# Performance work log

Hardware: AMD Instinct MI355X
Metric: run time of the kernel (lower is better)

The kernel has to match this reference:

```python
import jax, jax.numpy as jnp
import numpy as np

B, S, D_IN, D_H = 4, 2048, 1024, 1024


def setup_inputs() -> dict:
    key = jax.random.key(0)
    k1, k2, k3, k4, k5, k6 = jax.random.split(key, 6)
    seq1 = jax.random.normal(k1, (B, S, D_IN), dtype=jnp.float32)
    seq2 = jax.random.normal(k2, (B, S, D_IN), dtype=jnp.float32)
    attn_mask = jax.random.randint(k3, (B, S, S), 0, 2).astype(jnp.bool_)
    # nn.Linear weights: shape [out, in], y = x @ W^T
    scale = 1.0 / np.sqrt(D_IN)
    Wq = jax.random.uniform(k4, (D_H, D_IN), dtype=jnp.float32, minval=-scale, maxval=scale)
    Wk = jax.random.uniform(k5, (D_H, D_IN), dtype=jnp.float32, minval=-scale, maxval=scale)
    Wv = jax.random.uniform(k6, (D_H, D_IN), dtype=jnp.float32, minval=-scale, maxval=scale)
    return {"seq1": seq1, "seq2": seq2, "attn_mask": attn_mask, "Wq": Wq, "Wk": Wk, "Wv": Wv}


def reference(seq1, seq2, attn_mask, Wq, Wk, Wv):
    q = jnp.einsum('bsd,hd->bsh', seq1, Wq)
    k = jnp.einsum('bsd,hd->bsh', seq2, Wk)
    v = jnp.einsum('bsd,hd->bsh', seq2, Wv)
    score = jnp.einsum('bqh,bkh->bqk', q, k) / jnp.sqrt(jnp.float32(q.shape[-1]))
    # faithful to torch.masked_fill(..., value=1e-09): masked positions set to 1e-9
    mask_score = jnp.where(attn_mask, jnp.float32(1e-09), score)
    # faithful to torch.softmax(..., dim=1): softmax over the QUERY axis
    score_matrix = jax.nn.softmax(mask_score, axis=1)
    out = jnp.einsum('bqk,bkh->bqh', score_matrix, v)
    return out
```

## Files before the change

### kernel.cpp

```cpp
#include <hip/hip_runtime.h>

typedef __bf16 bx8 __attribute__((ext_vector_type(8)));
typedef __bf16 bx4 __attribute__((ext_vector_type(4)));
typedef float  fx4 __attribute__((ext_vector_type(4)));
typedef unsigned long long u64;

#define B_   4
#define S_   2048
#define DIN  1024
#define DH   1024

#define MB ((size_t)1 << 20)
#define WS_A1 ((size_t)0)
#define WS_A2 ((size_t)16*MB)
#define WS_PU ((size_t)0)
#define WS_WQ ((size_t)32*MB)
#define WS_BM ((size_t)38*MB)
#define WS_Q  ((size_t)40*MB)
#define WS_K  ((size_t)56*MB)
#define WS_VT ((size_t)72*MB)
#define WS_CS ((size_t)88*MB)

__global__ void cvt_seq(const float* __restrict__ s1, const float* __restrict__ s2,
                        __bf16* __restrict__ o1, __bf16* __restrict__ o2) {
  const float* in  = blockIdx.y ? s2 : s1;
  __bf16*      out = blockIdx.y ? o2 : o1;
  size_t i = (size_t)blockIdx.x * blockDim.x + threadIdx.x;
  fx4 lo = ((const fx4*)in)[2 * i];
  fx4 hi = ((const fx4*)in)[2 * i + 1];
  bx8 o;
#pragma unroll
  for (int j = 0; j < 4; j++) { o[j] = (__bf16)lo[j]; o[j + 4] = (__bf16)hi[j]; }
  ((bx8*)out)[i] = o;
}
__global__ void cvt_w(const float* __restrict__ wq, const float* __restrict__ wk,
                      const float* __restrict__ wv, __bf16* __restrict__ oq) {
  const float* in = blockIdx.y == 0 ? wq : (blockIdx.y == 1 ? wk : wv);
  __bf16* out = oq + (size_t)blockIdx.y * (DH * DIN);
  size_t i = (size_t)blockIdx.x * blockDim.x + threadIdx.x;
  fx4 lo = ((const fx4*)in)[2 * i];
  fx4 hi = ((const fx4*)in)[2 * i + 1];
  bx8 o;
#pragma unroll
  for (int j = 0; j < 4; j++) { o[j] = (__bf16)lo[j]; o[j + 4] = (__bf16)hi[j]; }
  ((bx8*)out)[i] = o;
}

__global__ void pack_mask(const int* __restrict__ m, u64* __restrict__ w) {
  const int wid = threadIdx.x >> 6, lane = threadIdx.x & 63;
  const size_t base = ((size_t)blockIdx.x * 4 + wid) * 512;
#pragma unroll
  for (int i = 0; i < 8; i++) {
    int v = m[base + i * 64 + lane];
    u64 b = __ballot(v != 0);
    if (lane == 0) w[base / 64 + i] = b;
  }
}


enum { EP_QKV = 0, EP_EXP = 2, EP_F32 = 3 };

#define GLD(gp, lp)                                                              \
  __builtin_amdgcn_global_load_lds(                                              \
      (const __attribute__((address_space(1))) void*)(const void*)(gp),          \
      (__attribute__((address_space(3))) void*)(void*)(lp), 16, 0, 0)

#define ENDSYNC()                                          \
  do {                                                     \
    asm volatile("s_waitcnt vmcnt(0)" ::: "memory");       \
    __builtin_amdgcn_s_barrier();                          \
    __builtin_amdgcn_sched_barrier(0);                     \
  } while (0)

#define MM(m, n, av, bv) \
  acc[m][n] = __builtin_amdgcn_mfma_f32_16x16x32_bf16(av, bv, acc[m][n], 0, 0, 0)

#define LDA_(bo, m, kk) (*(const bx8*)(aBase + (bo) + (m) * 2048 + ((kk) ? c1s : c0s)))
#define LDB_(bo, n, kk) (*(const bx8*)(bBase + (bo) + (n) * 2048 + ((kk) ? c1s : c0s)))

#define STAGE_A(kt, bo) do {                                              \
  GLD(pA + (kt),                    smem + (bo) + tid * 16);              \
  GLD(pA + (size_t)64 * K + (kt),   smem + (bo) + 8192 + tid * 16);       \
} while (0)
#define STAGE_B(kt, bo) do {                                              \
  GLD(pB + (kt),                    smem + (bo) + 16384 + tid * 16);      \
  GLD(pB + (size_t)64 * K + (kt),   smem + (bo) + 24576 + tid * 16);      \
} while (0)

template <int EPI>
__global__ __launch_bounds__(512, 4) void gemm128(
    const __bf16* __restrict__ A, const __bf16* __restrict__ Bm,
    void* __restrict__ Cout, void* __restrict__ Cout2,
    const void* __restrict__ Xtra, int N, int K, long sA, long sB) {
  extern __shared__ char smem[];

  int brow, bcol, bz = 0, qrow = 0;
  bool isQ = false;
  if (EPI == EP_QKV) {
    int f = (blockIdx.x & 7) * 192 + (blockIdx.x >> 3);
    if (f < 512) {
      isQ = true;
      qrow = (f >> 3) * 128;
      brow = qrow;
      bcol = (f & 7) * 128;
    } else {
      int g = f - 512;
      qrow = (g >> 4) * 128;
      brow = 8192 + qrow;
      bcol = (g & 15) * 128;
    }
  } else {
    const unsigned gx = gridDim.x, gy = gridDim.y;
    const unsigned nwg = gx * gy * gridDim.z;
    unsigned flat = (blockIdx.z * gy + blockIdx.y) * gx + blockIdx.x;
    flat = (flat & 7) * (nwg >> 3) + (flat >> 3);
    const int lx = __builtin_ctz(gx), ly = __builtin_ctz(gy);
    brow = ((flat >> lx) & (gy - 1)) * 128;
    bcol = (flat & (gx - 1)) * 128;
    bz   = flat >> (lx + ly);
    A  += (long)bz * sA;
    Bm += (long)bz * sB;
  }

  const int tid  = threadIdx.x;
  const int wid  = tid >> 6;
  const int lane = tid & 63;
  const int wr = wid >> 2;
  const int wc = wid & 3;

  fx4 acc[4][2] = {};

  const int gcol = (((tid & 7) ^ ((tid >> 3) & 7)) << 3);
  const __bf16* Bsel = (EPI == EP_QKV && !isQ) ? (Bm + (size_t)1048576) : Bm;
  const __bf16* pA = A    + (size_t)(brow + (tid >> 3)) * K + gcol;
  const __bf16* pB = Bsel + (size_t)(bcol + (tid >> 3)) * K + gcol;

  const int frow = lane & 15;
  const int slot = (lane >> 4) << 4;
  const int c0s  = slot ^ ((frow & 7) << 4);
  const int c1s  = (64 + slot) ^ ((frow & 7) << 4);
  const char* aBase = smem + (wr * 64 + frow) * 128;
  const char* bBase = smem + 16384 + (wc * 32 + frow) * 128;

  STAGE_A(0, 0); STAGE_B(0, 0);
  ENDSYNC();

  const int nt = K >> 6;
  int cur = 0, nb = 32768;
  bx8 a00, a01, a02, a03, a10, a11, a12, a13, b00, b01, b10, b11;

  for (int t = 0; t < nt; ++t) {
    const int k1 = (t + 1 < nt) ? (t + 1) * 64 : 0;

    STAGE_A(k1, nb); STAGE_B(k1, nb);

    a00 = LDA_(cur, 0, 0); a01 = LDA_(cur, 1, 0); a02 = LDA_(cur, 2, 0); a03 = LDA_(cur, 3, 0);
    b00 = LDB_(cur, 0, 0); b01 = LDB_(cur, 1, 0);
    a10 = LDA_(cur, 0, 1); a11 = LDA_(cur, 1, 1); a12 = LDA_(cur, 2, 1); a13 = LDA_(cur, 3, 1);
    b10 = LDB_(cur, 0, 1); b11 = LDB_(cur, 1, 1);

    __builtin_amdgcn_s_setprio(1);
    MM(0, 0, a00, b00); MM(0, 1, a00, b01);
    MM(1, 0, a01, b00); MM(1, 1, a01, b01);
    MM(2, 0, a02, b00); MM(2, 1, a02, b01);
    MM(3, 0, a03, b00); MM(3, 1, a03, b01);
    MM(0, 0, a10, b10); MM(0, 1, a10, b11);
    MM(1, 0, a11, b10); MM(1, 1, a11, b11);
    MM(2, 0, a12, b10); MM(2, 1, a12, b11);
    MM(3, 0, a13, b10); MM(3, 1, a13, b11);
    __builtin_amdgcn_s_setprio(0);

    ENDSYNC();
    int tmp = cur; cur = nb; nb = tmp;
  }

  const int r0 = wr * 64 + (lane >> 4) * 4;
  const int c0 = wc * 32 + (lane & 15);

  if (EPI == EP_QKV) {
    if (isQ) {
      __bf16* Cq = (__bf16*)Cout;
#pragma unroll
      for (int m = 0; m < 4; m++) {
        int row = qrow + r0 + m * 16;
#pragma unroll
        for (int n = 0; n < 2; n++) {
          int col = bcol + c0 + n * 16;
#pragma unroll
          for (int j = 0; j < 4; j++)
            Cq[(size_t)(row + j) * 1024 + col] = (__bf16)acc[m][n][j];
        }
      }
    } else if (bcol < 1024) {
      __bf16* Ck = (__bf16*)Cout2;
#pragma unroll
      for (int m = 0; m < 4; m++) {
        int rr = qrow + r0 + m * 16;
#pragma unroll
        for (int n = 0; n < 2; n++) {
          int col = bcol + c0 + n * 16;
#pragma unroll
          for (int j = 0; j < 4; j++)
            Ck[(size_t)(rr + j) * 1024 + col] = (__bf16)acc[m][n][j];
        }
      }
    } else {
      __bf16* Cv = (__bf16*)Xtra;
#pragma unroll
      for (int m = 0; m < 4; m++) {
        int rr = qrow + r0 + m * 16;
        size_t bb = (size_t)(rr >> 11) << 21;
        int sidx = rr & 2047;
#pragma unroll
        for (int n = 0; n < 2; n++) {
          int col = bcol + c0 + n * 16 - 1024;
          bx4 tv;
#pragma unroll
          for (int j = 0; j < 4; j++) tv[j] = (__bf16)acc[m][n][j];
          *(bx4*)&Cv[bb + (size_t)col * S_ + sidx] = tv;
        }
      }
    }
  } else if (EPI == EP_EXP) {
    __bf16* C     = (__bf16*)Cout + (size_t)bz * ((size_t)S_ * S_);
    const u64* Wm = (const u64*)Xtra + (((size_t)bz * S_ * S_) >> 6);
    float csum0 = 0.f, csum1 = 0.f;
#pragma unroll
    for (int m = 0; m < 4; m++) {
      int row = brow + r0 + m * 16;
#pragma unroll
      for (int n = 0; n < 2; n++) {
        int col = bcol + c0 + n * 16;
        float cl = 0.f;
#pragma unroll
        for (int j = 0; j < 4; j++) {
          size_t idx = (size_t)(row + j) * S_ + col;
          bool mk = (Wm[idx >> 6] >> (idx & 63)) & 1;
          float p = mk ? 1.0f : __expf(acc[m][n][j] * 0.03125f);
          cl += p;
          C[idx] = (__bf16)p;
        }
        if (n == 0) csum0 += cl; else csum1 += cl;
      }
    }
    csum0 += __shfl_xor(csum0, 16); csum0 += __shfl_xor(csum0, 32);
    csum1 += __shfl_xor(csum1, 16); csum1 += __shfl_xor(csum1, 32);
    if (lane < 16) {
      float* csp = (float*)Cout2 + (size_t)bz * S_ + bcol + wc * 32 + lane;
      atomicAdd(csp, csum0);
      atomicAdd(csp + 16, csum1);
    }
  } else {
    float* C = (float*)Cout + (size_t)bz * ((size_t)S_ * DH);
#pragma unroll
    for (int m = 0; m < 4; m++) {
      int row = brow + r0 + m * 16;
#pragma unroll
      for (int n = 0; n < 2; n++) {
        int col = bcol + c0 + n * 16;
#pragma unroll
        for (int j = 0; j < 4; j++)
          C[(size_t)(row + j) * N + col] = acc[m][n][j];
      }
    }
  }
}

__global__ void scale_vt(__bf16* __restrict__ vT, const float* __restrict__ cs) {
  size_t i = (size_t)blockIdx.x * blockDim.x + threadIdx.x;
  size_t e = i * 8;
  int b = (int)(e >> 21);
  int k = (int)(e & (S_ - 1));
  bx8 v = ((bx8*)vT)[i];
  const float* c = cs + (size_t)b * S_ + k;
#pragma unroll
  for (int j = 0; j < 8; j++) v[j] = (__bf16)((float)v[j] / c[j]);
  ((bx8*)vT)[i] = v;
}

extern "C" void kernel_launch(void* const* d_in, const int* in_sizes, int n_in,
                              void* d_out, int out_size, void* d_ws, size_t ws_size,
                              hipStream_t stream) {
  const float* seq1 = (const float*)d_in[0];
  const float* seq2 = (const float*)d_in[1];
  const int*   mask = (const int*)d_in[2];
  const float* Wq   = (const float*)d_in[3];
  const float* Wk   = (const float*)d_in[4];
  const float* Wv   = (const float*)d_in[5];

  char* ws = (char*)d_ws;
  __bf16* A1  = (__bf16*)(ws + WS_A1);
  __bf16* A2  = (__bf16*)(ws + WS_A2);
  __bf16* Pu  = (__bf16*)(ws + WS_PU);
  __bf16* WQb = (__bf16*)(ws + WS_WQ);
  u64*    bm  = (u64*)(ws + WS_BM);
  __bf16* qb  = (__bf16*)(ws + WS_Q);
  __bf16* kb  = (__bf16*)(ws + WS_K);
  __bf16* vTb = (__bf16*)(ws + WS_VT);
  float*  cs  = (float*)(ws + WS_CS);

  (void)hipFuncSetAttribute((const void*)gemm128<EP_QKV>,
      hipFuncAttributeMaxDynamicSharedMemorySize, 65536);
  (void)hipFuncSetAttribute((const void*)gemm128<EP_EXP>,
      hipFuncAttributeMaxDynamicSharedMemorySize, 65536);
  (void)hipFuncSetAttribute((const void*)gemm128<EP_F32>,
      hipFuncAttributeMaxDynamicSharedMemorySize, 65536);

  cvt_seq<<<dim3(4096, 2, 1), 256, 0, stream>>>(seq1, seq2, A1, A2);
  cvt_w<<<dim3(512, 3, 1), 256, 0, stream>>>(Wq, Wk, Wv, WQb);
  pack_mask<<<8192, 256, 0, stream>>>(mask, bm);
  hipMemsetAsync(ws + WS_CS, 0, (size_t)B_ * S_ * sizeof(float), stream);

  gemm128<EP_QKV><<<1536, 512, 65536, stream>>>(
      A1, WQb, qb, kb, vTb, 0, DIN, 0, 0);

  gemm128<EP_EXP><<<dim3(S_ / 128, S_ / 128, B_), 512, 65536, stream>>>(
      qb, kb, Pu, cs, bm, S_, DH, (long)S_ * DH, (long)S_ * DH);

  scale_vt<<<(B_ * DH * S_ / 8) / 256, 256, 0, stream>>>(vTb, cs);

  gemm128<EP_F32><<<dim3(DH / 128, S_ / 128, B_), 512, 65536, stream>>>(
      Pu, vTb, (float*)d_out, nullptr, nullptr, DH, S_, (long)S_ * S_, (long)DH * S_);
}
```

Before: 178.9 us.

## Fuse fp32-to-bf16 activation conversion and V column scaling into GEMM loaders

Removes the standalone cvt_seq and scale_vt kernels. The QKV GEMM now loads fp32 seq1/seq2 through registers, converts them to bf16 and writes them into LDS. The PV GEMM loads vT into registers, scales it by the reciprocal column sums, converts and stores it into LDS. This drops two extra passes over global memory and two launches. In exchange, those loads no longer use async global-to-LDS, they read twice the bytes for the A operand, and the loop waits on lgkmcnt, which may lengthen each iteration.

```diff
diff --git a/kernel.cpp b/kernel.cpp
--- a/kernel.cpp
+++ b/kernel.cpp
@@ -11,8 +11,6 @@
 #define DH   1024
 
 #define MB ((size_t)1 << 20)
-#define WS_A1 ((size_t)0)
-#define WS_A2 ((size_t)16*MB)
 #define WS_PU ((size_t)0)
 #define WS_WQ ((size_t)32*MB)
 #define WS_BM ((size_t)38*MB)
@@ -21,18 +19,6 @@
 #define WS_VT ((size_t)72*MB)
 #define WS_CS ((size_t)88*MB)
 
-__global__ void cvt_seq(const float* __restrict__ s1, const float* __restrict__ s2,
-                        __bf16* __restrict__ o1, __bf16* __restrict__ o2) {
-  const float* in  = blockIdx.y ? s2 : s1;
-  __bf16*      out = blockIdx.y ? o2 : o1;
-  size_t i = (size_t)blockIdx.x * blockDim.x + threadIdx.x;
-  fx4 lo = ((const fx4*)in)[2 * i];
-  fx4 hi = ((const fx4*)in)[2 * i + 1];
-  bx8 o;
-#pragma unroll
-  for (int j = 0; j < 4; j++) { o[j] = (__bf16)lo[j]; o[j + 4] = (__bf16)hi[j]; }
-  ((bx8*)out)[i] = o;
-}
 __global__ void cvt_w(const float* __restrict__ wq, const float* __restrict__ wk,
                       const float* __restrict__ wv, __bf16* __restrict__ oq) {
   const float* in = blockIdx.y == 0 ? wq : (blockIdx.y == 1 ? wk : wv);
@@ -65,11 +51,11 @@
       (const __attribute__((address_space(1))) void*)(const void*)(gp),          \
       (__attribute__((address_space(3))) void*)(void*)(lp), 16, 0, 0)
 
-#define ENDSYNC()                                          \
-  do {                                                     \
-    asm volatile("s_waitcnt vmcnt(0)" ::: "memory");       \
-    __builtin_amdgcn_s_barrier();                          \
-    __builtin_amdgcn_sched_barrier(0);                     \
+#define ENDSYNC()                                                      \
+  do {                                                                 \
+    asm volatile("s_waitcnt vmcnt(0) lgkmcnt(0)" ::: "memory");        \
+    __builtin_amdgcn_s_barrier();                                      \
+    __builtin_amdgcn_sched_barrier(0);                                 \
   } while (0)
 
 #define MM(m, n, av, bv) \
@@ -78,11 +64,11 @@
 #define LDA_(bo, m, kk) (*(const bx8*)(aBase + (bo) + (m) * 2048 + ((kk) ? c1s : c0s)))
 #define LDB_(bo, n, kk) (*(const bx8*)(bBase + (bo) + (n) * 2048 + ((kk) ? c1s : c0s)))
 
-#define STAGE_A(kt, bo) do {                                              \
+#define STAGE_A_GLD(kt, bo) do {                                          \
   GLD(pA + (kt),                    smem + (bo) + tid * 16);              \
   GLD(pA + (size_t)64 * K + (kt),   smem + (bo) + 8192 + tid * 16);       \
 } while (0)
-#define STAGE_B(kt, bo) do {                                              \
+#define STAGE_B_GLD(kt, bo) do {                                          \
   GLD(pB + (kt),                    smem + (bo) + 16384 + tid * 16);      \
   GLD(pB + (size_t)64 * K + (kt),   smem + (bo) + 24576 + tid * 16);      \
 } while (0)
@@ -91,7 +77,8 @@
 __global__ __launch_bounds__(512, 4) void gemm128(
     const __bf16* __restrict__ A, const __bf16* __restrict__ Bm,
     void* __restrict__ Cout, void* __restrict__ Cout2,
-    const void* __restrict__ Xtra, int N, int K, long sA, long sB) {
+    const void* __restrict__ Xtra, const float* __restrict__ F1,
+    const float* __restrict__ F2, int N, int K, long sA, long sB) {
   extern __shared__ char smem[];
 
   int brow, bcol, bz = 0, qrow = 0;
@@ -101,14 +88,13 @@
     if (f < 512) {
       isQ = true;
       qrow = (f >> 3) * 128;
-      brow = qrow;
       bcol = (f & 7) * 128;
     } else {
       int g = f - 512;
       qrow = (g >> 4) * 128;
-      brow = 8192 + qrow;
       bcol = (g & 15) * 128;
     }
+    brow = qrow;
   } else {
     const unsigned gx = gridDim.x, gy = gridDim.y;
     const unsigned nwg = gx * gy * gridDim.z;
@@ -132,8 +118,11 @@
 
   const int gcol = (((tid & 7) ^ ((tid >> 3) & 7)) << 3);
   const __bf16* Bsel = (EPI == EP_QKV && !isQ) ? (Bm + (size_t)1048576) : Bm;
-  const __bf16* pA = A    + (size_t)(brow + (tid >> 3)) * K + gcol;
-  const __bf16* pB = Bsel + (size_t)(bcol + (tid >> 3)) * K + gcol;
+  const __bf16* pA  = A    + (size_t)(brow + (tid >> 3)) * K + gcol;
+  const __bf16* pB  = Bsel + (size_t)(bcol + (tid >> 3)) * K + gcol;
+  const float*  pAf = (EPI == EP_QKV ? (isQ ? F1 : F2) : nullptr)
+                      + ((EPI == EP_QKV) ? ((size_t)(qrow + (tid >> 3)) * DIN + gcol) : 0);
+  const float*  csb = (EPI == EP_F32) ? (F1 + (size_t)bz * S_) : nullptr;
 
   const int frow = lane & 15;
   const int slot = (lane >> 4) << 4;
@@ -142,17 +131,63 @@
   const char* aBase = smem + (wr * 64 + frow) * 128;
   const char* bBase = smem + 16384 + (wc * 32 + frow) * 128;
 
-  STAGE_A(0, 0); STAGE_B(0, 0);
-  ENDSYNC();
-
   const int nt = K >> 6;
   int cur = 0, nb = 32768;
   bx8 a00, a01, a02, a03, a10, a11, a12, a13, b00, b01, b10, b11;
+  fx4 fa0, fa1, fa2, fa3;
+  bx8 lv0, lv1;
+  fx4 cs0, cs1;
+
+  if (EPI == EP_QKV) {
+    fa0 = *(const fx4*)(pAf);       fa1 = *(const fx4*)(pAf + 4);
+    fa2 = *(const fx4*)(pAf + (size_t)64 * DIN);
+    fa3 = *(const fx4*)(pAf + (size_t)64 * DIN + 4);
+    bx8 w0, w1;
+#pragma unroll
+    for (int j = 0; j < 4; j++) {
+      w0[j] = (__bf16)fa0[j]; w0[j + 4] = (__bf16)fa1[j];
+      w1[j] = (__bf16)fa2[j]; w1[j + 4] = (__bf16)fa3[j];
+    }
+    *(bx8*)(smem + tid * 16) = w0;
+    *(bx8*)(smem + 8192 + tid * 16) = w1;
+    STAGE_B_GLD(0, 0);
+  } else if (EPI == EP_F32) {
+    STAGE_A_GLD(0, 0);
+    lv0 = *(const bx8*)(pB);
+    lv1 = *(const bx8*)(pB + (size_t)64 * K);
+    cs0 = *(const fx4*)(csb + gcol);
+    cs1 = *(const fx4*)(csb + gcol + 4);
+    bx8 w0, w1;
+#pragma unroll
+    for (int j = 0; j < 8; j++) {
+      float r = __builtin_amdgcn_rcpf(j < 4 ? cs0[j] : cs1[j - 4]);
+      w0[j] = (__bf16)((float)lv0[j] * r);
+      w1[j] = (__bf16)((float)lv1[j] * r);
+    }
+    *(bx8*)(smem + 16384 + tid * 16) = w0;
+    *(bx8*)(smem + 24576 + tid * 16) = w1;
+  } else {
+    STAGE_A_GLD(0, 0); STAGE_B_GLD(0, 0);
+  }
+  ENDSYNC();
 
   for (int t = 0; t < nt; ++t) {
     const int k1 = (t + 1 < nt) ? (t + 1) * 64 : 0;
 
-    STAGE_A(k1, nb); STAGE_B(k1, nb);
+    if (EPI == EP_QKV) {
+      fa0 = *(const fx4*)(pAf + k1);     fa1 = *(const fx4*)(pAf + k1 + 4);
+      fa2 = *(const fx4*)(pAf + (size_t)64 * DIN + k1);
+      fa3 = *(const fx4*)(pAf + (size_t)64 * DIN + k1 + 4);
+      STAGE_B_GLD(k1, nb);
+    } else if (EPI == EP_F32) {
+      STAGE_A_GLD(k1, nb);
+      lv0 = *(const bx8*)(pB + k1);
+      lv1 = *(const bx8*)(pB + (size_t)64 * K + k1);
+      cs0 = *(const fx4*)(csb + k1 + gcol);
+      cs1 = *(const fx4*)(csb + k1 + gcol + 4);
+    } else {
+      STAGE_A_GLD(k1, nb); STAGE_B_GLD(k1, nb);
+    }
 
     a00 = LDA_(cur, 0, 0); a01 = LDA_(cur, 1, 0); a02 = LDA_(cur, 2, 0); a03 = LDA_(cur, 3, 0);
     b00 = LDB_(cur, 0, 0); b01 = LDB_(cur, 1, 0);
@@ -170,6 +205,27 @@
     MM(3, 0, a13, b10); MM(3, 1, a13, b11);
     __builtin_amdgcn_s_setprio(0);
 
+    if (EPI == EP_QKV) {
+      bx8 w0, w1;
+#pragma unroll
+      for (int j = 0; j < 4; j++) {
+        w0[j] = (__bf16)fa0[j]; w0[j + 4] = (__bf16)fa1[j];
+        w1[j] = (__bf16)fa2[j]; w1[j + 4] = (__bf16)fa3[j];
+      }
+      *(bx8*)(smem + nb + tid * 16) = w0;
+      *(bx8*)(smem + nb + 8192 + tid * 16) = w1;
+    } else if (EPI == EP_F32) {
+      bx8 w0, w1;
+#pragma unroll
+      for (int j = 0; j < 8; j++) {
+        float r = __builtin_amdgcn_rcpf(j < 4 ? cs0[j] : cs1[j - 4]);
+        w0[j] = (__bf16)((float)lv0[j] * r);
+        w1[j] = (__bf16)((float)lv1[j] * r);
+      }
+      *(bx8*)(smem + nb + 16384 + tid * 16) = w0;
+      *(bx8*)(smem + nb + 24576 + tid * 16) = w1;
+    }
+
     ENDSYNC();
     int tmp = cur; cur = nb; nb = tmp;
   }
@@ -264,18 +320,6 @@
       }
     }
   }
-}
-
-__global__ void scale_vt(__bf16* __restrict__ vT, const float* __restrict__ cs) {
-  size_t i = (size_t)blockIdx.x * blockDim.x + threadIdx.x;
-  size_t e = i * 8;
-  int b = (int)(e >> 21);
-  int k = (int)(e & (S_ - 1));
-  bx8 v = ((bx8*)vT)[i];
-  const float* c = cs + (size_t)b * S_ + k;
-#pragma unroll
-  for (int j = 0; j < 8; j++) v[j] = (__bf16)((float)v[j] / c[j]);
-  ((bx8*)vT)[i] = v;
 }
 
 extern "C" void kernel_launch(void* const* d_in, const int* in_sizes, int n_in,
@@ -289,8 +333,6 @@
   const float* Wv   = (const float*)d_in[5];
 
   char* ws = (char*)d_ws;
-  __bf16* A1  = (__bf16*)(ws + WS_A1);
-  __bf16* A2  = (__bf16*)(ws + WS_A2);
   __bf16* Pu  = (__bf16*)(ws + WS_PU);
   __bf16* WQb = (__bf16*)(ws + WS_WQ);
   u64*    bm  = (u64*)(ws + WS_BM);
@@ -306,19 +348,17 @@
   (void)hipFuncSetAttribute((const void*)gemm128<EP_F32>,
       hipFuncAttributeMaxDynamicSharedMemorySize, 65536);
 
-  cvt_seq<<<dim3(4096, 2, 1), 256, 0, stream>>>(seq1, seq2, A1, A2);
   cvt_w<<<dim3(512, 3, 1), 256, 0, stream>>>(Wq, Wk, Wv, WQb);
   pack_mask<<<8192, 256, 0, stream>>>(mask, bm);
   hipMemsetAsync(ws + WS_CS, 0, (size_t)B_ * S_ * sizeof(float), stream);
 
   gemm128<EP_QKV><<<1536, 512, 65536, stream>>>(
-      A1, WQb, qb, kb, vTb, 0, DIN, 0, 0);
+      nullptr, WQb, qb, kb, vTb, seq1, seq2, 0, DIN, 0, 0);
 
   gemm128<EP_EXP><<<dim3(S_ / 128, S_ / 128, B_), 512, 65536, stream>>>(
-      qb, kb, Pu, cs, bm, S_, DH, (long)S_ * DH, (long)S_ * DH);
-
-  scale_vt<<<(B_ * DH * S_ / 8) / 256, 256, 0, stream>>>(vTb, cs);
+      qb, kb, Pu, cs, bm, nullptr, nullptr, S_, DH, (long)S_ * DH, (long)S_ * DH);
 
   gemm128<EP_F32><<<dim3(DH / 128, S_ / 128, B_), 512, 65536, stream>>>(
-      Pu, vTb, (float*)d_out, nullptr, nullptr, DH, S_, (long)S_ * S_, (long)DH * S_);
+      Pu, vTb, (float*)d_out, nullptr, nullptr, cs, nullptr, DH, S_,
+      (long)S_ * S_, (long)DH * S_);
 }
```

Result: slower. 200.0 us (+11.8%).
